# Kernel optimization log

Measured on AMD Instinct MI355X. Metric: run time of the kernel, lower is better.

Reference implementation:

```python
import jax, jax.numpy as jnp
import numpy as np

IN_CH, OUT_CH, MINI = 1024, 1024, 8
GY, GX = OUT_CH // MINI, IN_CH // MINI  # 128, 128
BATCH = 32768


def setup_inputs() -> dict:
    key = jax.random.key(0)
    k1, k2 = jax.random.split(key)
    x = jax.random.normal(k1, (BATCH, IN_CH), dtype=jnp.float32)
    # kaiming-style init scale for the eigens parameter
    eigens = jax.random.normal(k2, (GY, GX, MINI), dtype=jnp.float32) * (2.0 / (GX * MINI)) ** 0.5
    return {"x": x, "eigens": eigens}


def reference(x, eigens):
    # Block-circulant linear: for each (y, x_blk) grid cell, circularly convolve
    # the length-MINI eigen vector with the corresponding input block, then sum
    # over input blocks. Done in the frequency domain (full FFT, matching
    # torch.rfft(..., onesided=False) + complex_mult + irfft in the original),
    # but with the redundant gridDim_y repeat fused into a complex einsum.
    gy, gx, k = eigens.shape
    xb = x.reshape(-1, gx, k)                      # [B, GX, K]
    f_e = jnp.fft.fft(eigens, axis=-1)             # [GY, GX, K] complex
    f_x = jnp.fft.fft(xb, axis=-1)                 # [B, GX, K] complex
    f_out = jnp.einsum('yxk,bxk->byk', f_e, f_x)   # elementwise mult + sum over GX
    out = jnp.fft.ifft(f_out, axis=-1).real.astype(x.dtype)  # [B, GY, K]
    return out.reshape(-1, gy * k)                 # [B, OUT_CH]
```

## Files before the change

### kernel.cpp

```cpp
#include <hip/hip_runtime.h>
#include <stdint.h>

#define M_BATCH 32768
#define N_OUT   1024
#define K_IN    1024

#define BM 128
#define BN 128
#define BK 64

typedef __attribute__((ext_vector_type(8))) short  short8;
typedef __attribute__((ext_vector_type(4))) float  f32x4;

__device__ __forceinline__ unsigned short f2bf(float f) {
    __bf16 h = (__bf16)f;
    return __builtin_bit_cast(unsigned short, h);
}

typedef const __attribute__((address_space(1))) unsigned int* gas_ptr;
typedef __attribute__((address_space(3))) unsigned int*       las_ptr;

__device__ __forceinline__ void gload_lds16(const void* g, void* l) {
    __builtin_amdgcn_global_load_lds((gas_ptr)g, (las_ptr)l, 16, 0, 0);
}

__global__ __launch_bounds__(256) void cvt_x(const float* __restrict__ x,
                                             unsigned short* __restrict__ xb) {
    const size_t total8 = (size_t)M_BATCH * K_IN / 8;
    const size_t stride = (size_t)gridDim.x * 256;
    for (size_t i = (size_t)blockIdx.x * 256 + threadIdx.x; i < total8; i += stride) {
        f32x4 v0 = *reinterpret_cast<const f32x4*>(x + i * 8);
        f32x4 v1 = *reinterpret_cast<const f32x4*>(x + i * 8 + 4);
        short8 b;
#pragma unroll
        for (int j = 0; j < 4; ++j) b[j]     = (short)f2bf(v0[j]);
#pragma unroll
        for (int j = 0; j < 4; ++j) b[j + 4] = (short)f2bf(v1[j]);
        *reinterpret_cast<short8*>(xb + i * 8) = b;
    }
}

__global__ __launch_bounds__(256) void build_w(const float* __restrict__ eig,
                                               unsigned short* __restrict__ W) {
    int tid = blockIdx.x * 256 + threadIdx.x;
    int y  = tid >> 7;
    int xb = tid & 127;
    const float* e = eig + (size_t)((y << 7) + xb) * 8;
    f32x4 e0 = *reinterpret_cast<const f32x4*>(e);
    f32x4 e1 = *reinterpret_cast<const f32x4*>(e + 4);
    float ev[8] = {e0[0], e0[1], e0[2], e0[3], e1[0], e1[1], e1[2], e1[3]};
#pragma unroll
    for (int j = 0; j < 8; ++j) {
        alignas(16) unsigned short wv[8];
#pragma unroll
        for (int c = 0; c < 8; ++c) wv[c] = f2bf(ev[(j - c) & 7]);
        *reinterpret_cast<uint4*>(W + (size_t)(y * 8 + j) * K_IN + xb * 8) =
            *reinterpret_cast<const uint4*>(wv);
    }
}

__global__ __launch_bounds__(256) void gemm_bf16(const unsigned short* __restrict__ A,
                                                 const unsigned short* __restrict__ W,
                                                 float* __restrict__ C) {
    __shared__ unsigned short Alds[BM * BK];
    __shared__ unsigned short Blds[BN * BK];

    const int bid  = blockIdx.x;
    const int swz  = (bid & 7) * 256 + (bid >> 3);
    const int nblk = swz & 7;
    const int mblk = swz >> 3;
    const int brow = mblk * BM;
    const int bcol = nblk * BN;

    const int tid  = threadIdx.x;
    const int lane = tid & 63;
    const int wv   = tid >> 6;
    const int wm   = wv >> 1;
    const int wn   = wv & 1;

    f32x4 acc[4][4];
    const f32x4 zero = {0.f, 0.f, 0.f, 0.f};
#pragma unroll
    for (int i = 0; i < 4; ++i)
#pragma unroll
        for (int j = 0; j < 4; ++j) acc[i][j] = zero;

    const int lrow = lane >> 3;
    const int lchk = (lane & 7) ^ lrow;
    const size_t arow0 = (size_t)(brow + wv * 32 + lrow);
    const size_t brow0 = (size_t)(bcol + wv * 32 + lrow);
    const unsigned short* Abase = A + arow0 * K_IN + lchk * 8;
    const unsigned short* Bbase = W + brow0 * K_IN + lchk * 8;
    unsigned short* AldsBase = Alds + wv * 2048;
    unsigned short* BldsBase = Blds + wv * 2048;

    for (int kt = 0; kt < K_IN; kt += BK) {
        __syncthreads();
#pragma unroll
        for (int s = 0; s < 4; ++s) {
            gload_lds16(Abase + (size_t)(s * 8) * K_IN + kt, AldsBase + s * 512);
            gload_lds16(Bbase + (size_t)(s * 8) * K_IN + kt, BldsBase + s * 512);
        }
        __syncthreads();
#pragma unroll
        for (int ks = 0; ks < 2; ++ks) {
            short8 af[4], bfr[4];
            const int cb = ks * 4 + (lane >> 4);
            const int sl = cb ^ (lane & 7);
#pragma unroll
            for (int mt = 0; mt < 4; ++mt) {
                int row = wm * 64 + mt * 16 + (lane & 15);
                af[mt] = *reinterpret_cast<const short8*>(Alds + row * BK + sl * 8);
            }
#pragma unroll
            for (int nt = 0; nt < 4; ++nt) {
                int row = wn * 64 + nt * 16 + (lane & 15);
                bfr[nt] = *reinterpret_cast<const short8*>(Blds + row * BK + sl * 8);
            }
#pragma unroll
            for (int mt = 0; mt < 4; ++mt)
#pragma unroll
                for (int nt = 0; nt < 4; ++nt)
                    acc[mt][nt] = __builtin_amdgcn_mfma_f32_16x16x32_bf16(
                        af[mt], bfr[nt], acc[mt][nt], 0, 0, 0);
        }
    }

#pragma unroll
    for (int mt = 0; mt < 4; ++mt) {
#pragma unroll
        for (int nt = 0; nt < 4; ++nt) {
            int col = bcol + wn * 64 + nt * 16 + (lane & 15);
#pragma unroll
            for (int r = 0; r < 4; ++r) {
                int row = brow + wm * 64 + mt * 16 + (lane >> 4) * 4 + r;
                C[(size_t)row * N_OUT + col] = acc[mt][nt][r];
            }
        }
    }
}

__global__ __launch_bounds__(256) void gemm_bt(const float* __restrict__ A,
                                               const unsigned short* __restrict__ W,
                                               float* __restrict__ C) {
    __shared__ unsigned short Alds[BM * BK];
    __shared__ unsigned short Blds[BN * BK];

    const int bid  = blockIdx.x;
    const int swz  = (bid & 7) * 256 + (bid >> 3);
    const int nblk = swz & 7;
    const int mblk = swz >> 3;
    const int brow = mblk * BM;
    const int bcol = nblk * BN;

    const int tid  = threadIdx.x;
    const int lane = tid & 63;
    const int wv   = tid >> 6;
    const int wm   = wv >> 1;
    const int wn   = wv & 1;

    f32x4 acc[4][4];
    const f32x4 zero = {0.f, 0.f, 0.f, 0.f};
#pragma unroll
    for (int i = 0; i < 4; ++i)
#pragma unroll
        for (int j = 0; j < 4; ++j) acc[i][j] = zero;

    const int srow  = tid >> 3;
    const int sslot = tid & 7;
    const int sk8   = sslot ^ (srow & 7);
    const float*          Abase = A + (size_t)(brow + srow) * K_IN + sk8 * 8;
    const unsigned short* Wbase = W + (size_t)(bcol + srow) * K_IN + sk8 * 8;
    unsigned short* AldsW = Alds + srow * BK + sslot * 8;
    unsigned short* BldsW = Blds + srow * BK + sslot * 8;

    for (int kt = 0; kt < K_IN; kt += BK) {
        __syncthreads();
#pragma unroll
        for (int it = 0; it < 4; ++it) {
            const float* src = Abase + (size_t)it * 32 * K_IN + kt;
            f32x4 v0 = *reinterpret_cast<const f32x4*>(src);
            f32x4 v1 = *reinterpret_cast<const f32x4*>(src + 4);
            short8 b;
#pragma unroll
            for (int i = 0; i < 4; ++i) b[i]     = (short)f2bf(v0[i]);
#pragma unroll
            for (int i = 0; i < 4; ++i) b[i + 4] = (short)f2bf(v1[i]);
            *reinterpret_cast<short8*>(AldsW + it * 32 * BK) = b;
        }
#pragma unroll
        for (int it = 0; it < 4; ++it) {
            const unsigned short* src = Wbase + (size_t)it * 32 * K_IN + kt;
            short8 b = *reinterpret_cast<const short8*>(src);
            *reinterpret_cast<short8*>(BldsW + it * 32 * BK) = b;
        }
        __syncthreads();
#pragma unroll
        for (int ks = 0; ks < 2; ++ks) {
            short8 af[4], bfr[4];
            const int cb = ks * 4 + (lane >> 4);
#pragma unroll
            for (int mt = 0; mt < 4; ++mt) {
                int row  = wm * 64 + mt * 16 + (lane & 15);
                int slot = cb ^ (row & 7);
                af[mt] = *reinterpret_cast<const short8*>(Alds + row * BK + slot * 8);
            }
#pragma unroll
            for (int nt = 0; nt < 4; ++nt) {
                int row  = wn * 64 + nt * 16 + (lane & 15);
                int slot = cb ^ (row & 7);
                bfr[nt] = *reinterpret_cast<const short8*>(Blds + row * BK + slot * 8);
            }
#pragma unroll
            for (int mt = 0; mt < 4; ++mt)
#pragma unroll
                for (int nt = 0; nt < 4; ++nt)
                    acc[mt][nt] = __builtin_amdgcn_mfma_f32_16x16x32_bf16(
                        af[mt], bfr[nt], acc[mt][nt], 0, 0, 0);
        }
    }

#pragma unroll
    for (int mt = 0; mt < 4; ++mt) {
#pragma unroll
        for (int nt = 0; nt < 4; ++nt) {
            int col = bcol + wn * 64 + nt * 16 + (lane & 15);
#pragma unroll
            for (int r = 0; r < 4; ++r) {
                int row = brow + wm * 64 + mt * 16 + (lane >> 4) * 4 + r;
                C[(size_t)row * N_OUT + col] = acc[mt][nt][r];
            }
        }
    }
}

extern "C" void kernel_launch(void* const* d_in, const int* in_sizes, int n_in,
                              void* d_out, int out_size, void* d_ws, size_t ws_size,
                              hipStream_t stream) {
    const float* x   = (const float*)d_in[0];
    const float* eig = (const float*)d_in[1];
    float* out = (float*)d_out;

    const size_t XB     = (size_t)M_BATCH * K_IN;
    const size_t W_ELTS = (size_t)N_OUT * K_IN;
    const size_t need   = XB * sizeof(unsigned short) + W_ELTS * sizeof(unsigned short);

    if (ws_size >= need) {
        unsigned short* xb = (unsigned short*)d_ws;
        unsigned short* W  = (unsigned short*)d_ws + XB;
        hipLaunchKernelGGL(cvt_x, dim3(2048), dim3(256), 0, stream, x, xb);
        hipLaunchKernelGGL(build_w, dim3(64), dim3(256), 0, stream, eig, W);
        hipLaunchKernelGGL(gemm_bf16, dim3((M_BATCH / BM) * (N_OUT / BN)), dim3(256),
                           0, stream, xb, W, out);
    } else if (ws_size >= W_ELTS * sizeof(unsigned short)) {
        unsigned short* W = (unsigned short*)d_ws;
        hipLaunchKernelGGL(build_w, dim3(64), dim3(256), 0, stream, eig, W);
        hipLaunchKernelGGL(gemm_bt, dim3((M_BATCH / BM) * (N_OUT / BN)), dim3(256),
                           0, stream, x, W, out);
    }
}
```

Baseline: 298.2 us.

## Replace bf16 GEMM with 256x256-tile, 4-stage pipelined async-LDS GEMM

Replaces the single-buffered 128x128 bf16 GEMM with a 512-thread kernel using 256x256 tiles, BK=32, and a four-deep ring of LDS buffers. Global-to-LDS loads are issued three stages ahead, with explicit vmcnt waits and a single barrier per iteration. MFMA blocks run under raised wave priority. This aims to hide global load latency and raise data reuse per tile. The cost is heavy register use for the 8x4 accumulators and 128KB of LDS, which may limit occupancy.

```diff
diff --git a/kernel.cpp b/kernel.cpp
--- a/kernel.cpp
+++ b/kernel.cpp
@@ -4,10 +4,6 @@
 #define M_BATCH 32768
 #define N_OUT   1024
 #define K_IN    1024
-
-#define BM 128
-#define BN 128
-#define BK 64
 
 typedef __attribute__((ext_vector_type(8))) short  short8;
 typedef __attribute__((ext_vector_type(4))) float  f32x4;
@@ -59,18 +55,132 @@
     }
 }
 
-__global__ __launch_bounds__(256) void gemm_bf16(const unsigned short* __restrict__ A,
-                                                 const unsigned short* __restrict__ W,
-                                                 float* __restrict__ C) {
-    __shared__ unsigned short Alds[BM * BK];
-    __shared__ unsigned short Blds[BN * BK];
+#define BM 256
+#define BN 256
+#define BK 32
+#define NT (K_IN / BK)
+
+__global__ __launch_bounds__(512, 2) void gemm_pipe(const unsigned short* __restrict__ A,
+                                                    const unsigned short* __restrict__ W,
+                                                    float* __restrict__ C) {
+    __shared__ unsigned short Alds[4][BM * BK];
+    __shared__ unsigned short Blds[4][BN * BK];
+
+    const int bid  = blockIdx.x;
+    const int swz  = (bid & 7) * 64 + (bid >> 3);
+    const int nblk = swz & 3;
+    const int mblk = swz >> 2;
+    const int brow = mblk * BM;
+    const int bcol = nblk * BN;
+
+    const int tid  = threadIdx.x;
+    const int lane = tid & 63;
+    const int w    = tid >> 6;
+    const int wm   = w >> 2;
+    const int wn   = w & 3;
+
+    const int srow   = lane >> 2;
+    const int schunk = (lane & 3) ^ ((lane >> 3) & 3);
+    const unsigned short* Ag0 = A + (size_t)(brow + w * 32 +  0 + srow) * K_IN + schunk * 8;
+    const unsigned short* Ag1 = A + (size_t)(brow + w * 32 + 16 + srow) * K_IN + schunk * 8;
+    const unsigned short* Bg0 = W + (size_t)(bcol + w * 32 +  0 + srow) * K_IN + schunk * 8;
+    const unsigned short* Bg1 = W + (size_t)(bcol + w * 32 + 16 + srow) * K_IN + schunk * 8;
+    const int ldsOff0 = (w * 32 +  0) * BK;
+    const int ldsOff1 = (w * 32 + 16) * BK;
+
+    auto stage = [&](int tt) {
+        const int b  = tt & 3;
+        const int kt = tt * BK;
+        gload_lds16(Ag0 + kt, &Alds[b][ldsOff0]);
+        gload_lds16(Ag1 + kt, &Alds[b][ldsOff1]);
+        gload_lds16(Bg0 + kt, &Blds[b][ldsOff0]);
+        gload_lds16(Bg1 + kt, &Blds[b][ldsOff1]);
+    };
+
+    f32x4 acc[8][4];
+    const f32x4 zero = {0.f, 0.f, 0.f, 0.f};
+#pragma unroll
+    for (int i = 0; i < 8; ++i)
+#pragma unroll
+        for (int j = 0; j < 4; ++j) acc[i][j] = zero;
+
+    const int kc   = lane >> 4;
+    const int slot = kc ^ ((lane >> 1) & 3);
+    const int arow = wm * 128 + (lane & 15);
+    const int brow_b = wn * 64 + (lane & 15);
+
+    auto compute = [&](int b) {
+        short8 bfr[4];
+#pragma unroll
+        for (int nt = 0; nt < 4; ++nt)
+            bfr[nt] = *reinterpret_cast<const short8*>(
+                &Blds[b][(brow_b + nt * 16) * BK + slot * 8]);
+        short8 af[8];
+#pragma unroll
+        for (int mt = 0; mt < 8; ++mt)
+            af[mt] = *reinterpret_cast<const short8*>(
+                &Alds[b][(arow + mt * 16) * BK + slot * 8]);
+        __builtin_amdgcn_s_setprio(1);
+#pragma unroll
+        for (int mt = 0; mt < 8; ++mt)
+#pragma unroll
+            for (int nt = 0; nt < 4; ++nt)
+                acc[mt][nt] = __builtin_amdgcn_mfma_f32_16x16x32_bf16(
+                    af[mt], bfr[nt], acc[mt][nt], 0, 0, 0);
+        __builtin_amdgcn_s_setprio(0);
+    };
+
+    stage(0); stage(1); stage(2);
+    asm volatile("s_waitcnt vmcnt(8)" ::: "memory");
+    __builtin_amdgcn_s_barrier();
+    __builtin_amdgcn_sched_barrier(0);
+
+    for (int t = 0; t < NT - 3; ++t) {
+        stage(t + 3);
+        compute(t & 3);
+        asm volatile("s_waitcnt vmcnt(8)" ::: "memory");
+        __builtin_amdgcn_s_barrier();
+        __builtin_amdgcn_sched_barrier(0);
+    }
+    compute((NT - 3) & 3);
+    asm volatile("s_waitcnt vmcnt(4)" ::: "memory");
+    __builtin_amdgcn_s_barrier();
+    __builtin_amdgcn_sched_barrier(0);
+    compute((NT - 2) & 3);
+    asm volatile("s_waitcnt vmcnt(0)" ::: "memory");
+    __builtin_amdgcn_s_barrier();
+    __builtin_amdgcn_sched_barrier(0);
+    compute((NT - 1) & 3);
+
+#pragma unroll
+    for (int mt = 0; mt < 8; ++mt) {
+#pragma unroll
+        for (int nt = 0; nt < 4; ++nt) {
+            int col = bcol + wn * 64 + nt * 16 + (lane & 15);
+#pragma unroll
+            for (int r = 0; r < 4; ++r) {
+                int row = brow + wm * 128 + mt * 16 + (lane >> 4) * 4 + r;
+                C[(size_t)row * N_OUT + col] = acc[mt][nt][r];
+            }
+        }
+    }
+}
+
+#define FBM 128
+#define FBN 128
+#define FBK 64
+__global__ __launch_bounds__(256) void gemm_bt(const float* __restrict__ A,
+                                               const unsigned short* __restrict__ W,
+                                               float* __restrict__ C) {
+    __shared__ unsigned short Alds[FBM * FBK];
+    __shared__ unsigned short Blds[FBN * FBK];
 
     const int bid  = blockIdx.x;
     const int swz  = (bid & 7) * 256 + (bid >> 3);
     const int nblk = swz & 7;
     const int mblk = swz >> 3;
-    const int brow = mblk * BM;
-    const int bcol = nblk * BN;
+    const int brow = mblk * FBM;
+    const int bcol = nblk * FBN;
 
     const int tid  = threadIdx.x;
     const int lane = tid & 63;
@@ -85,96 +195,15 @@
 #pragma unroll
         for (int j = 0; j < 4; ++j) acc[i][j] = zero;
 
-    const int lrow = lane >> 3;
-    const int lchk = (lane & 7) ^ lrow;
-    const size_t arow0 = (size_t)(brow + wv * 32 + lrow);
-    const size_t brow0 = (size_t)(bcol + wv * 32 + lrow);
-    const unsigned short* Abase = A + arow0 * K_IN + lchk * 8;
-    const unsigned short* Bbase = W + brow0 * K_IN + lchk * 8;
-    unsigned short* AldsBase = Alds + wv * 2048;
-    unsigned short* BldsBase = Blds + wv * 2048;
-
-    for (int kt = 0; kt < K_IN; kt += BK) {
-        __syncthreads();
-#pragma unroll
-        for (int s = 0; s < 4; ++s) {
-            gload_lds16(Abase + (size_t)(s * 8) * K_IN + kt, AldsBase + s * 512);
-            gload_lds16(Bbase + (size_t)(s * 8) * K_IN + kt, BldsBase + s * 512);
-        }
-        __syncthreads();
-#pragma unroll
-        for (int ks = 0; ks < 2; ++ks) {
-            short8 af[4], bfr[4];
-            const int cb = ks * 4 + (lane >> 4);
-            const int sl = cb ^ (lane & 7);
-#pragma unroll
-            for (int mt = 0; mt < 4; ++mt) {
-                int row = wm * 64 + mt * 16 + (lane & 15);
-                af[mt] = *reinterpret_cast<const short8*>(Alds + row * BK + sl * 8);
-            }
-#pragma unroll
-            for (int nt = 0; nt < 4; ++nt) {
-                int row = wn * 64 + nt * 16 + (lane & 15);
-                bfr[nt] = *reinterpret_cast<const short8*>(Blds + row * BK + sl * 8);
-            }
-#pragma unroll
-            for (int mt = 0; mt < 4; ++mt)
-#pragma unroll
-                for (int nt = 0; nt < 4; ++nt)
-                    acc[mt][nt] = __builtin_amdgcn_mfma_f32_16x16x32_bf16(
-                        af[mt], bfr[nt], acc[mt][nt], 0, 0, 0);
-        }
-    }
-
-#pragma unroll
-    for (int mt = 0; mt < 4; ++mt) {
-#pragma unroll
-        for (int nt = 0; nt < 4; ++nt) {
-            int col = bcol + wn * 64 + nt * 16 + (lane & 15);
-#pragma unroll
-            for (int r = 0; r < 4; ++r) {
-                int row = brow + wm * 64 + mt * 16 + (lane >> 4) * 4 + r;
-                C[(size_t)row * N_OUT + col] = acc[mt][nt][r];
-            }
-        }
-    }
-}
-
-__global__ __launch_bounds__(256) void gemm_bt(const float* __restrict__ A,
-                                               const unsigned short* __restrict__ W,
-                                               float* __restrict__ C) {
-    __shared__ unsigned short Alds[BM * BK];
-    __shared__ unsigned short Blds[BN * BK];
-
-    const int bid  = blockIdx.x;
-    const int swz  = (bid & 7) * 256 + (bid >> 3);
-    const int nblk = swz & 7;
-    const int mblk = swz >> 3;
-    const int brow = mblk * BM;
-    const int bcol = nblk * BN;
-
-    const int tid  = threadIdx.x;
-    const int lane = tid & 63;
-    const int wv   = tid >> 6;
-    const int wm   = wv >> 1;
-    const int wn   = wv & 1;
-
-    f32x4 acc[4][4];
-    const f32x4 zero = {0.f, 0.f, 0.f, 0.f};
-#pragma unroll
-    for (int i = 0; i < 4; ++i)
-#pragma unroll
-        for (int j = 0; j < 4; ++j) acc[i][j] = zero;
-
     const int srow  = tid >> 3;
     const int sslot = tid & 7;
     const int sk8   = sslot ^ (srow & 7);
     const float*          Abase = A + (size_t)(brow + srow) * K_IN + sk8 * 8;
     const unsigned short* Wbase = W + (size_t)(bcol + srow) * K_IN + sk8 * 8;
-    unsigned short* AldsW = Alds + srow * BK + sslot * 8;
-    unsigned short* BldsW = Blds + srow * BK + sslot * 8;
-
-    for (int kt = 0; kt < K_IN; kt += BK) {
+    unsigned short* AldsW = Alds + srow * FBK + sslot * 8;
+    unsigned short* BldsW = Blds + srow * FBK + sslot * 8;
+
+    for (int kt = 0; kt < K_IN; kt += FBK) {
         __syncthreads();
 #pragma unroll
         for (int it = 0; it < 4; ++it) {
@@ -186,13 +215,13 @@
             for (int i = 0; i < 4; ++i) b[i]     = (short)f2bf(v0[i]);
 #pragma unroll
             for (int i = 0; i < 4; ++i) b[i + 4] = (short)f2bf(v1[i]);
-            *reinterpret_cast<short8*>(AldsW + it * 32 * BK) = b;
+            *reinterpret_cast<short8*>(AldsW + it * 32 * FBK) = b;
         }
 #pragma unroll
         for (int it = 0; it < 4; ++it) {
             const unsigned short* src = Wbase + (size_t)it * 32 * K_IN + kt;
             short8 b = *reinterpret_cast<const short8*>(src);
-            *reinterpret_cast<short8*>(BldsW + it * 32 * BK) = b;
+            *reinterpret_cast<short8*>(BldsW + it * 32 * FBK) = b;
         }
         __syncthreads();
 #pragma unroll
@@ -203,13 +232,13 @@
             for (int mt = 0; mt < 4; ++mt) {
                 int row  = wm * 64 + mt * 16 + (lane & 15);
                 int slot = cb ^ (row & 7);
-                af[mt] = *reinterpret_cast<const short8*>(Alds + row * BK + slot * 8);
+                af[mt] = *reinterpret_cast<const short8*>(Alds + row * FBK + slot * 8);
             }
 #pragma unroll
             for (int nt = 0; nt < 4; ++nt) {
                 int row  = wn * 64 + nt * 16 + (lane & 15);
                 int slot = cb ^ (row & 7);
-                bfr[nt] = *reinterpret_cast<const short8*>(Blds + row * BK + slot * 8);
+                bfr[nt] = *reinterpret_cast<const short8*>(Blds + row * FBK + slot * 8);
             }
 #pragma unroll
             for (int mt = 0; mt < 4; ++mt)
@@ -243,19 +272,19 @@
 
     const size_t XB     = (size_t)M_BATCH * K_IN;
     const size_t W_ELTS = (size_t)N_OUT * K_IN;
-    const size_t need   = XB * sizeof(unsigned short) + W_ELTS * sizeof(unsigned short);
+    const size_t need   = (XB + W_ELTS) * sizeof(unsigned short);
 
     if (ws_size >= need) {
         unsigned short* xb = (unsigned short*)d_ws;
         unsigned short* W  = (unsigned short*)d_ws + XB;
+        hipLaunchKernelGGL(build_w, dim3(64), dim3(256), 0, stream, eig, W);
         hipLaunchKernelGGL(cvt_x, dim3(2048), dim3(256), 0, stream, x, xb);
-        hipLaunchKernelGGL(build_w, dim3(64), dim3(256), 0, stream, eig, W);
-        hipLaunchKernelGGL(gemm_bf16, dim3((M_BATCH / BM) * (N_OUT / BN)), dim3(256),
+        hipLaunchKernelGGL(gemm_pipe, dim3((M_BATCH / BM) * (N_OUT / BN)), dim3(512),
                            0, stream, xb, W, out);
     } else if (ws_size >= W_ELTS * sizeof(unsigned short)) {
         unsigned short* W = (unsigned short*)d_ws;
         hipLaunchKernelGGL(build_w, dim3(64), dim3(256), 0, stream, eig, W);
-        hipLaunchKernelGGL(gemm_bt, dim3((M_BATCH / BM) * (N_OUT / BN)), dim3(256),
+        hipLaunchKernelGGL(gemm_bt, dim3((M_BATCH / FBM) * (N_OUT / FBN)), dim3(256),
                            0, stream, x, W, out);
     }
 }
```

After: 312.5 us. +4.8%, slower.
